# Kernel tuning notes

Measured on AMD Instinct MI355X. Metric: run time of the kernel, lower is better.

Reference implementation:

```python
import jax, jax.numpy as jnp
import numpy as np


def setup_inputs() -> dict:
    key = jax.random.key(0)
    ks = jax.random.split(key, 8)
    H, O, B, T = 1024, 512, 512, 256
    s_ih = 1.0 / np.sqrt(H)
    return {
        "h0": jax.random.normal(ks[0], (1, B, H), jnp.float32),
        "c0": jax.random.normal(ks[1], (1, B, H), jnp.float32),
        "W_ih": jax.random.normal(ks[2], (4 * H, O), jnp.float32) * s_ih,
        "W_hh": jax.random.normal(ks[3], (4 * H, H), jnp.float32) * s_ih,
        "b_ih": jax.random.normal(ks[4], (4 * H,), jnp.float32) * s_ih,
        "b_hh": jax.random.normal(ks[5], (4 * H,), jnp.float32) * s_ih,
        "W_out": jax.random.normal(ks[6], (O, H), jnp.float32) * s_ih,
        "b_out": jax.random.normal(ks[7], (O,), jnp.float32) * s_ih,
        "out_len": T,
    }


def reference(h0, c0, W_ih, W_hh, b_ih, b_hh, W_out, b_out, out_len):
    B = h0.shape[1]
    O = W_out.shape[0]
    h = h0.reshape(B, -1)  # [B, H]
    c = c0.reshape(B, -1)  # [B, H]
    x = jnp.zeros((B, O), dtype=h.dtype)  # initial lstm_in of zeros

    def step(carry, _):
        h, c, x = carry
        # PyTorch LSTMCell: gates ordered (i, f, g, o)
        gates = x @ W_ih.T + b_ih + h @ W_hh.T + b_hh  # [B, 4H]
        i, f, g, o = jnp.split(gates, 4, axis=-1)
        c_new = jax.nn.sigmoid(f) * c + jax.nn.sigmoid(i) * jnp.tanh(g)
        h_new = jax.nn.sigmoid(o) * jnp.tanh(c_new)
        y = jax.nn.softmax(h_new @ W_out.T + b_out, axis=-1)  # [B, O]
        return (h_new, c_new, y), y

    _, ys = jax.lax.scan(step, (h, c, x), None, length=out_len)
    # original writes output[i-1] for i = out_len..1, i.e. time-reversed storage
    return ys[::-1]  # [out_len, B, O]
```

## Files before the change

kernel.cpp:

```cpp
#include <hip/hip_runtime.h>
#include <math.h>

#define BB 512
#define HH 1024
#define OO 512
#define KC 1536
#define G4H 4096
#define TT 256

typedef _Float16 half8 __attribute__((ext_vector_type(8)));
typedef float f32x4 __attribute__((ext_vector_type(4)));

__device__ __forceinline__ void dma16(const void* g, void* l) {
    __builtin_amdgcn_global_load_lds(
        (const __attribute__((address_space(1))) void*)g,
        (__attribute__((address_space(3))) void*)l, 16, 0, 0);
}

__global__ __launch_bounds__(256) void conv_wcat(
    const float* __restrict__ W_ih, const float* __restrict__ W_hh,
    _Float16* __restrict__ Wcat)
{
    int k = blockIdx.x * 256 + threadIdx.x;
    int p = blockIdx.y;
    int g = (p >> 5) & 3, jt = p >> 7, jr = p & 31;
    int n = g * HH + jt * 32 + jr;
    float v = (k < OO) ? W_ih[(size_t)n * OO + k] : W_hh[(size_t)n * HH + (k - OO)];
    Wcat[(size_t)p * KC + k] = (_Float16)v;
}

__global__ __launch_bounds__(256) void conv_wout(
    const float* __restrict__ W_out, _Float16* __restrict__ Wout16)
{
    int k = blockIdx.x * 256 + threadIdx.x;
    int o = blockIdx.y;
    Wout16[(size_t)o * HH + k] = (_Float16)W_out[(size_t)o * HH + k];
}

__global__ __launch_bounds__(256) void prep_misc(
    const float* __restrict__ b_ih, const float* __restrict__ b_hh,
    const float* __restrict__ h0, const float* __restrict__ c0,
    float* __restrict__ bias_p, _Float16* __restrict__ xh0, float* __restrict__ cst)
{
    int idx0 = blockIdx.x * blockDim.x + threadIdx.x;
    int stride = gridDim.x * blockDim.x;
    for (int p = idx0; p < G4H; p += stride) {
        int g = (p >> 5) & 3, jt = p >> 7, jr = p & 31;
        int n = g * HH + jt * 32 + jr;
        bias_p[p] = b_ih[n] + b_hh[n];
    }
    for (int i = idx0; i < BB * KC; i += stride) {
        int b = i / KC, q = i - b * KC;
        xh0[i] = (q < OO) ? (_Float16)0.f : (_Float16)h0[b * HH + (q - OO)];
    }
    for (int i = idx0; i < BB * HH; i += stride) cst[i] = c0[i];
}

__global__ __launch_bounds__(256) void gates_mfma(
    const _Float16* __restrict__ xh_in,
    _Float16* __restrict__ xh_out,
    float* __restrict__ cst,
    const _Float16* __restrict__ Wcat,
    const float* __restrict__ bias_p)
{
    const int pt = blockIdx.x;
    const int p0 = pt * 128, b0 = blockIdx.y * 64;
    const int tid = threadIdx.x;
    const int l = tid & 63, w = tid >> 6;
    const int wm = w & 1, wn = w >> 1;
    const int l15 = l & 15, l4 = l >> 4;

    __shared__ __align__(16) char smem[49152];
    _Float16* Af = (_Float16*)smem;
    _Float16* Bf = (_Float16*)(smem + 16384);

    f32x4 acc[2][4];
    #pragma unroll
    for (int fm = 0; fm < 2; ++fm)
        #pragma unroll
        for (int fn = 0; fn < 4; ++fn)
            acc[fm][fn] = (f32x4){0.f, 0.f, 0.f, 0.f};

    half8 ra[4], rb[8];

    auto load_regs = [&](int k0) {
        #pragma unroll
        for (int j = 0; j < 4; ++j) {
            int row = (w * 4 + j) * 4 + l4;
            int c = l15 ^ (row & 7);
            ra[j] = *(const half8*)&xh_in[(size_t)(b0 + row) * KC + k0 + c * 8];
        }
        #pragma unroll
        for (int j = 0; j < 8; ++j) {
            int row = (w * 8 + j) * 4 + l4;
            int c = l15 ^ (row & 7);
            rb[j] = *(const half8*)&Wcat[(size_t)(p0 + row) * KC + k0 + c * 8];
        }
    };
    auto store_lds = [&]() {
        #pragma unroll
        for (int j = 0; j < 4; ++j)
            *(half8*)&Af[(size_t)(w * 4 + j) * 512 + l * 8] = ra[j];
        #pragma unroll
        for (int j = 0; j < 8; ++j)
            *(half8*)&Bf[(size_t)(w * 8 + j) * 512 + l * 8] = rb[j];
    };

    load_regs(0);
    #pragma unroll 1
    for (int it = 0; it < KC / 128; ++it) {
        __syncthreads();
        store_lds();
        __syncthreads();
        if (it + 1 < KC / 128) load_regs((it + 1) * 128);

        #pragma unroll
        for (int ks = 0; ks < 4; ++ks) {
            int cc = (ks * 4 + l4) ^ (l15 & 7);
            half8 af[2], bfr[4];
            #pragma unroll
            for (int fm = 0; fm < 2; ++fm) {
                int R = wm * 32 + fm * 16 + l15;
                af[fm] = *(const half8*)&Af[R * 128 + cc * 8];
            }
            #pragma unroll
            for (int fn = 0; fn < 4; ++fn) {
                int S = wn * 64 + fn * 16 + l15;
                bfr[fn] = *(const half8*)&Bf[S * 128 + cc * 8];
            }
            #pragma unroll
            for (int fm = 0; fm < 2; ++fm)
                #pragma unroll
                for (int fn = 0; fn < 4; ++fn)
                    acc[fm][fn] = __builtin_amdgcn_mfma_f32_16x16x32_f16(
                        af[fm], bfr[fn], acc[fm][fn], 0, 0, 0);
        }
    }
    __syncthreads();

    float* exch = (float*)smem;
    #pragma unroll
    for (int fm = 0; fm < 2; ++fm)
        #pragma unroll
        for (int fn = 0; fn < 4; ++fn)
            #pragma unroll
            for (int r = 0; r < 4; ++r) {
                int row = wm * 32 + fm * 16 + l4 * 4 + r;
                int col = wn * 64 + fn * 16 + l15;
                exch[row * 133 + col] = acc[fm][fn][r];
            }
    __syncthreads();

    int bl = tid >> 2;
    int b = b0 + bl;
    int jbase = (tid & 3) * 8;
    float cv[8], hv[8], cold[8];
    *(float4*)&cold[0] = *(const float4*)&cst[(size_t)b * HH + pt * 32 + jbase];
    *(float4*)&cold[4] = *(const float4*)&cst[(size_t)b * HH + pt * 32 + jbase + 4];
    #pragma unroll
    for (int u = 0; u < 8; ++u) {
        int jr = jbase + u;
        float gi = exch[bl * 133 +       jr] + bias_p[p0 +       jr];
        float gf = exch[bl * 133 + 32 + jr] + bias_p[p0 + 32 + jr];
        float gg = exch[bl * 133 + 64 + jr] + bias_p[p0 + 64 + jr];
        float go = exch[bl * 133 + 96 + jr] + bias_p[p0 + 96 + jr];
        float iv = 1.f / (1.f + expf(-gi));
        float fv = 1.f / (1.f + expf(-gf));
        float gv = tanhf(gg);
        float ov = 1.f / (1.f + expf(-go));
        float cnew = fv * cold[u] + iv * gv;
        cv[u] = cnew;
        hv[u] = ov * tanhf(cnew);
    }
    *(float4*)&cst[(size_t)b * HH + pt * 32 + jbase]     = *(const float4*)&cv[0];
    *(float4*)&cst[(size_t)b * HH + pt * 32 + jbase + 4] = *(const float4*)&cv[4];
    half8 hh;
    #pragma unroll
    for (int u = 0; u < 8; ++u) hh[u] = (_Float16)hv[u];
    *(half8*)&xh_out[(size_t)b * KC + OO + pt * 32 + jbase] = hh;
}

__global__ __launch_bounds__(128) void logits_mfma(
    const _Float16* __restrict__ xh,
    const _Float16* __restrict__ Wout16,
    const float* __restrict__ b_out,
    float* __restrict__ logits)
{
    const int o0 = blockIdx.x * 32, b0 = blockIdx.y * 32;
    const int tid = threadIdx.x;
    const int l = tid & 63, w = tid >> 6;
    const int l15 = l & 15, l4 = l >> 4, lo3 = l & 7;

    __shared__ __align__(16) _Float16 Ah[32 * 128];
    __shared__ __align__(16) _Float16 Bo[32 * 128];

    f32x4 acc[2];
    acc[0] = (f32x4){0.f, 0.f, 0.f, 0.f};
    acc[1] = (f32x4){0.f, 0.f, 0.f, 0.f};

    for (int k0 = 0; k0 < HH; k0 += 128) {
        #pragma unroll
        for (int j = 0; j < 4; ++j) {
            int row = (w * 4 + j) * 4 + l4;
            int c = l15 ^ (row & 7);
            dma16(&xh[(size_t)(b0 + row) * KC + OO + k0 + c * 8],
                  &Ah[(size_t)(w * 4 + j) * 512]);
        }
        #pragma unroll
        for (int j = 0; j < 4; ++j) {
            int row = (w * 4 + j) * 4 + l4;
            int c = l15 ^ (row & 7);
            dma16(&Wout16[(size_t)(o0 + row) * HH + k0 + c * 8],
                  &Bo[(size_t)(w * 4 + j) * 512]);
        }
        __syncthreads();
        #pragma unroll
        for (int ks = 0; ks < 4; ++ks) {
            int cc = (ks * 4 + l4) ^ lo3;
            int R = w * 16 + l15;
            half8 a = *(const half8*)&Ah[R * 128 + cc * 8];
            #pragma unroll
            for (int fn = 0; fn < 2; ++fn) {
                int S = fn * 16 + l15;
                half8 bq = *(const half8*)&Bo[S * 128 + cc * 8];
                acc[fn] = __builtin_amdgcn_mfma_f32_16x16x32_f16(a, bq, acc[fn], 0, 0, 0);
            }
        }
        __syncthreads();
    }
    #pragma unroll
    for (int fn = 0; fn < 2; ++fn)
        #pragma unroll
        for (int r = 0; r < 4; ++r) {
            int row = b0 + w * 16 + l4 * 4 + r;
            int col = o0 + fn * 16 + l15;
            logits[(size_t)row * OO + col] = acc[fn][r] + b_out[col];
        }
}

__global__ __launch_bounds__(256) void softmax_kernel(
    const float* __restrict__ logits,
    float* __restrict__ out_slice, _Float16* __restrict__ xh_next)
{
    const int w = threadIdx.x >> 6, l = threadIdx.x & 63;
    const int b = blockIdx.x * 4 + w;
    float v[8];
    *(float4*)&v[0] = *(const float4*)&logits[(size_t)b * OO + l * 8];
    *(float4*)&v[4] = *(const float4*)&logits[(size_t)b * OO + l * 8 + 4];

    float m = v[0];
    #pragma unroll
    for (int u = 1; u < 8; ++u) m = fmaxf(m, v[u]);
    #pragma unroll
    for (int off = 1; off < 64; off <<= 1) m = fmaxf(m, __shfl_xor(m, off, 64));

    float s = 0.f;
    #pragma unroll
    for (int u = 0; u < 8; ++u) { v[u] = expf(v[u] - m); s += v[u]; }
    #pragma unroll
    for (int off = 1; off < 64; off <<= 1) s += __shfl_xor(s, off, 64);

    float inv = 1.f / s;
    float y[8];
    half8 hh;
    #pragma unroll
    for (int u = 0; u < 8; ++u) { y[u] = v[u] * inv; hh[u] = (_Float16)y[u]; }
    *(float4*)&out_slice[(size_t)b * OO + l * 8]     = *(const float4*)&y[0];
    *(float4*)&out_slice[(size_t)b * OO + l * 8 + 4] = *(const float4*)&y[4];
    *(half8*)&xh_next[(size_t)b * KC + l * 8] = hh;
}

extern "C" void kernel_launch(void* const* d_in, const int* in_sizes, int n_in,
                              void* d_out, int out_size, void* d_ws, size_t ws_size,
                              hipStream_t stream)
{
    const float* h0    = (const float*)d_in[0];
    const float* c0    = (const float*)d_in[1];
    const float* W_ih  = (const float*)d_in[2];
    const float* W_hh  = (const float*)d_in[3];
    const float* b_ih  = (const float*)d_in[4];
    const float* b_hh  = (const float*)d_in[5];
    const float* W_out = (const float*)d_in[6];
    const float* b_out = (const float*)d_in[7];
    float* out = (float*)d_out;

    char* wsb = (char*)d_ws;
    _Float16* Wcat   = (_Float16*)wsb;                 wsb += (size_t)G4H * KC * 2;
    _Float16* Wout16 = (_Float16*)wsb;                 wsb += (size_t)OO * HH * 2;
    float*    bias_p = (float*)wsb;                    wsb += (size_t)G4H * 4;
    _Float16* xh0    = (_Float16*)wsb;                 wsb += (size_t)BB * KC * 2;
    _Float16* xh1    = (_Float16*)wsb;                 wsb += (size_t)BB * KC * 2;
    float*    cst    = (float*)wsb;                    wsb += (size_t)BB * HH * 4;
    float*    logits = (float*)wsb;                    wsb += (size_t)BB * OO * 4;

    conv_wcat<<<dim3(KC / 256, G4H), 256, 0, stream>>>(W_ih, W_hh, Wcat);
    conv_wout<<<dim3(HH / 256, OO), 256, 0, stream>>>(W_out, Wout16);
    prep_misc<<<512, 256, 0, stream>>>(b_ih, b_hh, h0, c0, bias_p, xh0, cst);

    for (int t = 0; t < TT; ++t) {
        _Float16* xin  = (t & 1) ? xh1 : xh0;
        _Float16* xout = (t & 1) ? xh0 : xh1;
        gates_mfma<<<dim3(32, 8), 256, 0, stream>>>(xin, xout, cst, Wcat, bias_p);
        logits_mfma<<<dim3(16, 16), 128, 0, stream>>>(xout, Wout16, b_out, logits);
        softmax_kernel<<<128, 256, 0, stream>>>(
            logits, out + (size_t)(TT - 1 - t) * BB * OO, xout);
    }
}
```

Baseline: 7.317 ms.

## Fuse softmax of previous step into gates kernel and skip zero input at t=0

Removes the per-step softmax kernel by having the gates kernel compute row max and inverse sum from the previous step's logits, then rebuild the fp16 softmax input on the fly while loading the A tile. Blocks with pt==0 also write the probability output slice, and a final softmax kernel produces the last output. At the first step the zero input columns are skipped by starting the K loop later. This cuts one launch per step and the xh round trip. In exchange, each of the 32 column blocks recomputes the softmax statistics and exponentials redundantly.

Measured after the change: 11.80 ms. 1.61x slower.

```diff
diff --git a/kernel.cpp b/kernel.cpp
--- a/kernel.cpp
+++ b/kernel.cpp
@@ -40,7 +40,7 @@
 __global__ __launch_bounds__(256) void prep_misc(
     const float* __restrict__ b_ih, const float* __restrict__ b_hh,
     const float* __restrict__ h0, const float* __restrict__ c0,
-    float* __restrict__ bias_p, _Float16* __restrict__ xh0, float* __restrict__ cst)
+    float* __restrict__ bias_p, _Float16* __restrict__ hb0, float* __restrict__ cst)
 {
     int idx0 = blockIdx.x * blockDim.x + threadIdx.x;
     int stride = gridDim.x * blockDim.x;
@@ -49,19 +49,21 @@
         int n = g * HH + jt * 32 + jr;
         bias_p[p] = b_ih[n] + b_hh[n];
     }
-    for (int i = idx0; i < BB * KC; i += stride) {
-        int b = i / KC, q = i - b * KC;
-        xh0[i] = (q < OO) ? (_Float16)0.f : (_Float16)h0[b * HH + (q - OO)];
-    }
-    for (int i = idx0; i < BB * HH; i += stride) cst[i] = c0[i];
-}
-
-__global__ __launch_bounds__(256) void gates_mfma(
-    const _Float16* __restrict__ xh_in,
-    _Float16* __restrict__ xh_out,
+    for (int i = idx0; i < BB * HH; i += stride) {
+        hb0[i] = (_Float16)h0[i];
+        cst[i] = c0[i];
+    }
+}
+
+__global__ __launch_bounds__(256) void gates_sf(
+    const float* __restrict__ logits,
+    const _Float16* __restrict__ h_in,
+    _Float16* __restrict__ h_out,
     float* __restrict__ cst,
     const _Float16* __restrict__ Wcat,
-    const float* __restrict__ bias_p)
+    const float* __restrict__ bias_p,
+    float* __restrict__ out_slice,
+    int first)
 {
     const int pt = blockIdx.x;
     const int p0 = pt * 128, b0 = blockIdx.y * 64;
@@ -70,9 +72,46 @@
     const int wm = w & 1, wn = w >> 1;
     const int l15 = l & 15, l4 = l >> 4;
 
-    __shared__ __align__(16) char smem[49152];
+    __shared__ __align__(16) char smem[49664];
     _Float16* Af = (_Float16*)smem;
     _Float16* Bf = (_Float16*)(smem + 16384);
+    float* sm_m   = (float*)(smem + 49152);
+    float* sm_inv = (float*)(smem + 49408);
+
+    if (!first) {
+        #pragma unroll 1
+        for (int rr = 0; rr < 16; ++rr) {
+            int bl = w * 16 + rr;
+            const float* lr = &logits[(size_t)(b0 + bl) * OO];
+            float v[8];
+            *(float4*)&v[0] = *(const float4*)&lr[l * 8];
+            *(float4*)&v[4] = *(const float4*)&lr[l * 8 + 4];
+
+            float m = v[0];
+            #pragma unroll
+            for (int u = 1; u < 8; ++u) m = fmaxf(m, v[u]);
+            #pragma unroll
+            for (int off = 1; off < 64; off <<= 1) m = fmaxf(m, __shfl_xor(m, off, 64));
+
+            float s = 0.f;
+            #pragma unroll
+            for (int u = 0; u < 8; ++u) { v[u] = expf(v[u] - m); s += v[u]; }
+            #pragma unroll
+            for (int off = 1; off < 64; off <<= 1) s += __shfl_xor(s, off, 64);
+
+            float inv = 1.f / s;
+            if (l == 0) { sm_m[bl] = m; sm_inv[bl] = inv; }
+            if (pt == 0) {
+                float y[8];
+                #pragma unroll
+                for (int u = 0; u < 8; ++u) y[u] = v[u] * inv;
+                float* os = &out_slice[(size_t)(b0 + bl) * OO];
+                *(float4*)&os[l * 8]     = *(const float4*)&y[0];
+                *(float4*)&os[l * 8 + 4] = *(const float4*)&y[4];
+            }
+        }
+    }
+    __syncthreads();
 
     f32x4 acc[2][4];
     #pragma unroll
@@ -84,11 +123,27 @@
     half8 ra[4], rb[8];
 
     auto load_regs = [&](int k0) {
-        #pragma unroll
-        for (int j = 0; j < 4; ++j) {
-            int row = (w * 4 + j) * 4 + l4;
-            int c = l15 ^ (row & 7);
-            ra[j] = *(const half8*)&xh_in[(size_t)(b0 + row) * KC + k0 + c * 8];
+        if (k0 < OO) {
+            #pragma unroll
+            for (int j = 0; j < 4; ++j) {
+                int row = (w * 4 + j) * 4 + l4;
+                int c = l15 ^ (row & 7);
+                const float* lp = &logits[(size_t)(b0 + row) * OO + k0 + c * 8];
+                float lv[8];
+                *(float4*)&lv[0] = *(const float4*)lp;
+                *(float4*)&lv[4] = *(const float4*)(lp + 4);
+                float m = sm_m[row], inv = sm_inv[row];
+                #pragma unroll
+                for (int e = 0; e < 8; ++e)
+                    ra[j][e] = (_Float16)(expf(lv[e] - m) * inv);
+            }
+        } else {
+            #pragma unroll
+            for (int j = 0; j < 4; ++j) {
+                int row = (w * 4 + j) * 4 + l4;
+                int c = l15 ^ (row & 7);
+                ra[j] = *(const half8*)&h_in[(size_t)(b0 + row) * HH + (k0 - OO) + c * 8];
+            }
         }
         #pragma unroll
         for (int j = 0; j < 8; ++j) {
@@ -106,9 +161,10 @@
             *(half8*)&Bf[(size_t)(w * 8 + j) * 512 + l * 8] = rb[j];
     };
 
-    load_regs(0);
+    const int it0 = first ? 4 : 0;
+    load_regs(it0 * 128);
     #pragma unroll 1
-    for (int it = 0; it < KC / 128; ++it) {
+    for (int it = it0; it < KC / 128; ++it) {
         __syncthreads();
         store_lds();
         __syncthreads();
@@ -160,7 +216,7 @@
     #pragma unroll
     for (int u = 0; u < 8; ++u) {
         int jr = jbase + u;
-        float gi = exch[bl * 133 +       jr] + bias_p[p0 +       jr];
+        float gi = exch[bl * 133 +      jr] + bias_p[p0 +      jr];
         float gf = exch[bl * 133 + 32 + jr] + bias_p[p0 + 32 + jr];
         float gg = exch[bl * 133 + 64 + jr] + bias_p[p0 + 64 + jr];
         float go = exch[bl * 133 + 96 + jr] + bias_p[p0 + 96 + jr];
@@ -177,11 +233,11 @@
     half8 hh;
     #pragma unroll
     for (int u = 0; u < 8; ++u) hh[u] = (_Float16)hv[u];
-    *(half8*)&xh_out[(size_t)b * KC + OO + pt * 32 + jbase] = hh;
+    *(half8*)&h_out[(size_t)b * HH + pt * 32 + jbase] = hh;
 }
 
 __global__ __launch_bounds__(128) void logits_mfma(
-    const _Float16* __restrict__ xh,
+    const _Float16* __restrict__ hb,
     const _Float16* __restrict__ Wout16,
     const float* __restrict__ b_out,
     float* __restrict__ logits)
@@ -203,7 +259,7 @@
         for (int j = 0; j < 4; ++j) {
             int row = (w * 4 + j) * 4 + l4;
             int c = l15 ^ (row & 7);
-            dma16(&xh[(size_t)(b0 + row) * KC + OO + k0 + c * 8],
+            dma16(&hb[(size_t)(b0 + row) * HH + k0 + c * 8],
                   &Ah[(size_t)(w * 4 + j) * 512]);
         }
         #pragma unroll
@@ -238,9 +294,8 @@
         }
 }
 
-__global__ __launch_bounds__(256) void softmax_kernel(
-    const float* __restrict__ logits,
-    float* __restrict__ out_slice, _Float16* __restrict__ xh_next)
+__global__ __launch_bounds__(256) void softmax_out(
+    const float* __restrict__ logits, float* __restrict__ out_slice)
 {
     const int w = threadIdx.x >> 6, l = threadIdx.x & 63;
     const int b = blockIdx.x * 4 + w;
@@ -262,12 +317,10 @@
 
     float inv = 1.f / s;
     float y[8];
-    half8 hh;
-    #pragma unroll
-    for (int u = 0; u < 8; ++u) { y[u] = v[u] * inv; hh[u] = (_Float16)y[u]; }
+    #pragma unroll
+    for (int u = 0; u < 8; ++u) y[u] = v[u] * inv;
     *(float4*)&out_slice[(size_t)b * OO + l * 8]     = *(const float4*)&y[0];
     *(float4*)&out_slice[(size_t)b * OO + l * 8 + 4] = *(const float4*)&y[4];
-    *(half8*)&xh_next[(size_t)b * KC + l * 8] = hh;
 }
 
 extern "C" void kernel_launch(void* const* d_in, const int* in_sizes, int n_in,
@@ -288,21 +341,22 @@
     _Float16* Wcat   = (_Float16*)wsb;                 wsb += (size_t)G4H * KC * 2;
     _Float16* Wout16 = (_Float16*)wsb;                 wsb += (size_t)OO * HH * 2;
     float*    bias_p = (float*)wsb;                    wsb += (size_t)G4H * 4;
-    _Float16* xh0    = (_Float16*)wsb;                 wsb += (size_t)BB * KC * 2;
-    _Float16* xh1    = (_Float16*)wsb;                 wsb += (size_t)BB * KC * 2;
+    _Float16* hb0    = (_Float16*)wsb;                 wsb += (size_t)BB * HH * 2;
+    _Float16* hb1    = (_Float16*)wsb;                 wsb += (size_t)BB * HH * 2;
     float*    cst    = (float*)wsb;                    wsb += (size_t)BB * HH * 4;
     float*    logits = (float*)wsb;                    wsb += (size_t)BB * OO * 4;
 
     conv_wcat<<<dim3(KC / 256, G4H), 256, 0, stream>>>(W_ih, W_hh, Wcat);
     conv_wout<<<dim3(HH / 256, OO), 256, 0, stream>>>(W_out, Wout16);
-    prep_misc<<<512, 256, 0, stream>>>(b_ih, b_hh, h0, c0, bias_p, xh0, cst);
+    prep_misc<<<512, 256, 0, stream>>>(b_ih, b_hh, h0, c0, bias_p, hb0, cst);
 
     for (int t = 0; t < TT; ++t) {
-        _Float16* xin  = (t & 1) ? xh1 : xh0;
-        _Float16* xout = (t & 1) ? xh0 : xh1;
-        gates_mfma<<<dim3(32, 8), 256, 0, stream>>>(xin, xout, cst, Wcat, bias_p);
-        logits_mfma<<<dim3(16, 16), 128, 0, stream>>>(xout, Wout16, b_out, logits);
-        softmax_kernel<<<128, 256, 0, stream>>>(
-            logits, out + (size_t)(TT - 1 - t) * BB * OO, xout);
-    }
-}
+        _Float16* hin  = (t & 1) ? hb1 : hb0;
+        _Float16* hout = (t & 1) ? hb0 : hb1;
+        float* oslice = (t == 0) ? out : out + (size_t)(TT - t) * BB * OO;
+        gates_sf<<<dim3(32, 8), 256, 0, stream>>>(
+            logits, hin, hout, cst, Wcat, bias_p, oslice, (t == 0) ? 1 : 0);
+        logits_mfma<<<dim3(16, 16), 128, 0, stream>>>(hout, Wout16, b_out, logits);
+    }
+    softmax_out<<<128, 256, 0, stream>>>(logits, out);
+}
```
